# Kernel tuning notes

Hardware: AMD Instinct MI355X
Metric: run time of the kernel (lower is better)

## Reference

```python
import jax, jax.numpy as jnp
import numpy as np

T, B, N = 512, 256, 128


def setup_inputs() -> dict:
    key = jax.random.key(0)
    k1, k2, k3, k4, k5, k6 = jax.random.split(key, 6)
    emit = jax.random.normal(k1, (T, B, N), dtype=jnp.float32)
    target = jax.random.randint(k2, (T, B), 0, N, dtype=jnp.int32)
    # monotone mask: each sequence has length in [T//2, T]
    lengths = jax.random.randint(k3, (B,), T // 2, T + 1, dtype=jnp.int32)
    mask = jnp.arange(T, dtype=jnp.int32)[:, None] < lengths[None, :]
    trans = 0.1 * jax.random.normal(k4, (N, N), dtype=jnp.float32)
    strans = 0.1 * jax.random.normal(k5, (N,), dtype=jnp.float32)
    etrans = 0.1 * jax.random.normal(k6, (N,), dtype=jnp.float32)
    return {"emit": emit, "target": target, "mask": mask,
            "trans": trans, "strans": strans, "etrans": etrans}


def _crf_nll(emit, trans, strans, etrans, target, mask):
    t_len, b, n = emit.shape

    # ---- logZ: forward algorithm (sequential scan over time) ----
    def step(alpha, inp):
        emit_i, mask_i = inp  # [B,N], [B]
        # scores[b, j, k] = alpha[b, j] + trans[j, k] + emit_i[b, k]
        scores = jax.nn.logsumexp(
            alpha[:, :, None] + trans[None, :, :] + emit_i[:, None, :], axis=1)
        alpha = jnp.where(mask_i[:, None], scores, alpha)
        return alpha, None

    alpha0 = strans[None, :] + emit[0]  # [B,N]
    alpha, _ = jax.lax.scan(step, alpha0, (emit[1:], mask[1:]))
    logZ = jax.nn.logsumexp(alpha + etrans[None, :], axis=1).sum()

    # ---- gold score ----
    emit_sc = jnp.take_along_axis(emit, target[:, :, None], axis=2)[..., 0]  # [T,B]
    trans_sc = trans[target[:-1], target[1:]]  # [T-1,B]
    scores = emit_sc.at[1:].add(trans_sc)
    score = jnp.where(mask, scores, 0.0).sum()
    ends = mask.sum(axis=0) - 1  # [B]
    score = score + strans[target[0]].sum()
    score = score + etrans[target[ends, jnp.arange(b)]].sum()

    return (logZ - score) / b


def reference(emit, target, mask, trans, strans, etrans):
    return _crf_nll(emit, trans, strans, etrans, target, mask)
```

## Files before the change

### kernel.cpp

```cpp
#include <hip/hip_runtime.h>

#define T_LEN 512
#define B_SZ  256
#define N_ST  128

#if defined(__has_builtin)
# if __has_builtin(__builtin_amdgcn_fdot2_f32_bf16)
#  define HAVE_DOT2 1
# endif
#endif
#ifndef HAVE_DOT2
# define HAVE_DOT2 0
#endif

typedef unsigned int uint32;
typedef __bf16 bf16x2 __attribute__((ext_vector_type(2)));
typedef float f2v __attribute__((ext_vector_type(2)));
typedef uint4 __attribute__((may_alias)) uint4a;

__device__ __forceinline__ uint32 bf16rn(float f) {
    uint32 u = __builtin_bit_cast(uint32, f);
    u += 0x7fffu + ((u >> 16) & 1u);
    return u >> 16;
}
__device__ __forceinline__ uint32 pack2(float lo, float hi) {
    return bf16rn(lo) | (bf16rn(hi) << 16);
}
__device__ __forceinline__ uint32 cvtpk(float lo, float hi) {
    uint32 r;
    asm("v_cvt_pk_bf16_f32 %0, %1, %2" : "=v"(r) : "v"(lo), "v"(hi));
    return r;
}
__device__ __forceinline__ float readlane0(float v) {
    return __builtin_bit_cast(float, (uint32)__builtin_amdgcn_readlane(__builtin_bit_cast(int, v), 0));
}
__device__ __forceinline__ float dot2b(uint32 a, uint32 b, float c) {
#if HAVE_DOT2
    return __builtin_amdgcn_fdot2_f32_bf16(__builtin_bit_cast(bf16x2, a),
                                           __builtin_bit_cast(bf16x2, b), c, false);
#else
    float alo = __builtin_bit_cast(float, a << 16);
    float ahi = __builtin_bit_cast(float, a & 0xffff0000u);
    float blo = __builtin_bit_cast(float, b << 16);
    float bhi = __builtin_bit_cast(float, b & 0xffff0000u);
    return fmaf(ahi, bhi, fmaf(alo, blo, c));
#endif
}


__global__ __launch_bounds__(64) void lengths_kernel(const unsigned char* __restrict__ mask_raw,
                                                     int* __restrict__ lens) {
    int b = blockIdx.x;
    int l = threadIdx.x;
    unsigned char b1 = mask_raw[1], b2 = mask_raw[2];
    int mode = (b1 != 0) ? 0 : ((b2 != 0) ? 2 : 1);
    int cnt = 0;
    if (mode == 0) {
        #pragma unroll
        for (int k = 0; k < 8; ++k) cnt += (mask_raw[(l * 8 + k) * B_SZ + b] != 0);
    } else if (mode == 1) {
        const int* m = (const int*)mask_raw;
        #pragma unroll
        for (int k = 0; k < 8; ++k) cnt += (m[(l * 8 + k) * B_SZ + b] != 0);
    } else {
        const float* m = (const float*)mask_raw;
        #pragma unroll
        for (int k = 0; k < 8; ++k) cnt += (m[(l * 8 + k) * B_SZ + b] != 0.0f);
    }
    #pragma unroll
    for (int off = 1; off < 64; off <<= 1) cnt += __shfl_xor(cnt, off);
    if (l == 0) lens[b] = cnt;
}

__global__ void __attribute__((amdgpu_flat_work_group_size(128, 128), amdgpu_waves_per_eu(1, 1)))
forward_kernel(
        const float* __restrict__ emit,
        const float* __restrict__ trans,
        const float* __restrict__ strans,
        const float* __restrict__ etrans,
        const int* __restrict__ lens,
        float* __restrict__ logZ_out) {
    const int b   = blockIdx.x;
    const int tid = threadIdx.x;
    const int wid = tid >> 6;
    const int l   = tid & 63;
    const int c0  = 2 * l, c1 = 2 * l + 1;

    __shared__ alignas(16) uint32 a32[64];
    __shared__ alignas(16) uint32 z32[64];
    __shared__ float meetA[N_ST], meetY[N_ST];
    __shared__ float maccSh[2], red2[2];

    const int len = lens[b];
    const int m = (len - 1 < 256) ? (len - 1) : 256;
    const float* eb = emit + (size_t)b * N_ST;
    const size_t TS2 = (size_t)B_SZ * N_ST / 2;
    const f2v* ebv = (const f2v*)eb;

    if (wid == 0) {
        uint32 EA[64], EB[64];
        #pragma unroll
        for (int p = 0; p < 64; ++p) {
            EA[p] = pack2(__expf(trans[(2 * p) * N_ST + c0]), __expf(trans[(2 * p + 1) * N_ST + c0]));
            EB[p] = pack2(__expf(trans[(2 * p) * N_ST + c1]), __expf(trans[(2 * p + 1) * N_ST + c1]));
        }
        float aA = __expf(strans[c0] + eb[c0]);
        float aB = __expf(strans[c1] + eb[c1]);
        a32[l] = pack2(aA, aB);
        float Macc = 0.f, inv = 1.0f;
        #define EIDX(T) ((size_t)(((T) <= m) ? (T) : m) * TS2 + l)
        f2v p0 = ebv[EIDX(1)];
        f2v p1 = ebv[EIDX(2)];
        f2v p2 = ebv[EIDX(3)];
        f2v p3 = ebv[EIDX(4)];
        for (int t = 1; t <= m; ++t) {
            const f2v pn = ebv[EIDX(t + 4)];
            const float ee0 = __expf(p0.x), ee1 = __expf(p0.y);
            float A0 = 0, A1 = 0, A2 = 0, A3 = 0, B0 = 0, B1 = 0, B2 = 0, B3 = 0;
            const uint4a* aw = (const uint4a*)a32;
            #pragma unroll
            for (int q = 0; q < 16; ++q) {
                const uint4 w = aw[q];
                A0 = dot2b(w.x, EA[4 * q + 0], A0);  B0 = dot2b(w.x, EB[4 * q + 0], B0);
                A1 = dot2b(w.y, EA[4 * q + 1], A1);  B1 = dot2b(w.y, EB[4 * q + 1], B1);
                A2 = dot2b(w.z, EA[4 * q + 2], A2);  B2 = dot2b(w.z, EB[4 * q + 2], B2);
                A3 = dot2b(w.w, EA[4 * q + 3], A3);  B3 = dot2b(w.w, EB[4 * q + 3], B3);
            }
            const float rA = (A0 + A1) + (A2 + A3);
            const float rB = (B0 + B1) + (B2 + B3);
            Macc -= __logf(inv);
            aA = ee0 * rA * inv;
            aB = ee1 * rB * inv;
            a32[l] = cvtpk(aA, aB);
            inv = __builtin_amdgcn_rcpf(readlane0(rA));
            p0 = p1; p1 = p2; p2 = p3; p3 = pn;
        }
        #undef EIDX
        meetA[c0] = aA; meetA[c1] = aB;
        if (l == 0) maccSh[0] = Macc;
    } else {
        uint32 RA[64], RB[64];
        #pragma unroll
        for (int p = 0; p < 64; ++p) {
            RA[p] = pack2(__expf(trans[c0 * N_ST + 2 * p]), __expf(trans[c0 * N_ST + 2 * p + 1]));
            RB[p] = pack2(__expf(trans[c1 * N_ST + 2 * p]), __expf(trans[c1 * N_ST + 2 * p + 1]));
        }
        float y0 = __expf(etrans[c0]);
        float y1 = __expf(etrans[c1]);
        float Maccb = 0.f, invb = 1.0f;
        const int t0 = len - 1;
        #define EIDXB(T) ((size_t)(((T) > m) ? (T) : (m + 1)) * TS2 + l)
        f2v p0 = ebv[EIDXB(t0)];
        f2v p1 = ebv[EIDXB(t0 - 1)];
        f2v p2 = ebv[EIDXB(t0 - 2)];
        f2v p3 = ebv[EIDXB(t0 - 3)];
        for (int t = t0; t > m; --t) {
            const f2v pn = ebv[EIDXB(t - 4)];
            const float ee0 = __expf(p0.x), ee1 = __expf(p0.y);
            z32[l] = cvtpk(ee0 * y0, ee1 * y1);
            float R0 = 0, R1 = 0, R2 = 0, R3 = 0, S0 = 0, S1 = 0, S2 = 0, S3 = 0;
            const uint4a* zw = (const uint4a*)z32;
            #pragma unroll
            for (int q = 0; q < 16; ++q) {
                const uint4 w = zw[q];
                R0 = dot2b(w.x, RA[4 * q + 0], R0);  S0 = dot2b(w.x, RB[4 * q + 0], S0);
                R1 = dot2b(w.y, RA[4 * q + 1], R1);  S1 = dot2b(w.y, RB[4 * q + 1], S1);
                R2 = dot2b(w.z, RA[4 * q + 2], R2);  S2 = dot2b(w.z, RB[4 * q + 2], S2);
                R3 = dot2b(w.w, RA[4 * q + 3], R3);  S3 = dot2b(w.w, RB[4 * q + 3], S3);
            }
            const float rR = (R0 + R1) + (R2 + R3);
            const float rS = (S0 + S1) + (S2 + S3);
            Maccb -= __logf(invb);
            y0 = rR * invb;
            y1 = rS * invb;
            invb = __builtin_amdgcn_rcpf(readlane0(rR));
            p0 = p1; p1 = p2; p2 = p3; p3 = pn;
        }
        #undef EIDXB
        meetY[c0] = y0; meetY[c1] = y1;
        if (l == 0) maccSh[1] = Maccb;
    }

    __syncthreads();
    float v = meetA[tid] * meetY[tid];
    #pragma unroll
    for (int off = 1; off < 64; off <<= 1) v += __shfl_xor(v, off);
    if (l == 0) red2[wid] = v;
    __syncthreads();
    if (tid == 0) logZ_out[b] = maccSh[0] + maccSh[1] + __logf(red2[0] + red2[1]);
}

__global__ __launch_bounds__(128) void score_kernel(
        const float* __restrict__ emit,
        const int* __restrict__ target,
        const float* __restrict__ trans,
        const float* __restrict__ strans,
        const float* __restrict__ etrans,
        const int* __restrict__ lens,
        float* __restrict__ score_out) {
    const int b   = blockIdx.x;
    const int tid = threadIdx.x;
    const int len = lens[b];
    float local = 0.f;
    for (int t = tid; t < len; t += 128) {
        int tgt = target[t * B_SZ + b];
        float v = emit[(size_t)t * (B_SZ * N_ST) + b * N_ST + tgt];
        if (t > 0) v += trans[target[(t - 1) * B_SZ + b] * N_ST + tgt];
        local += v;
    }
    if (tid == 0) {
        local += strans[target[b]];
        local += etrans[target[(len - 1) * B_SZ + b]];
    }
    #pragma unroll
    for (int off = 1; off < 64; off <<= 1) local += __shfl_xor(local, off);
    __shared__ float partial[2];
    if ((tid & 63) == 0) partial[tid >> 6] = local;
    __syncthreads();
    if (tid == 0) score_out[b] = partial[0] + partial[1];
}

__global__ __launch_bounds__(256) void finalize_kernel(
        const float* __restrict__ logZ,
        const float* __restrict__ score,
        float* __restrict__ out) {
    int tid = threadIdx.x;
    float v = logZ[tid] - score[tid];
    #pragma unroll
    for (int off = 1; off < 64; off <<= 1) v += __shfl_xor(v, off);
    __shared__ float p[4];
    if ((tid & 63) == 0) p[tid >> 6] = v;
    __syncthreads();
    if (tid == 0) out[0] = (p[0] + p[1] + p[2] + p[3]) / 256.0f;
}

extern "C" void kernel_launch(void* const* d_in, const int* in_sizes, int n_in,
                              void* d_out, int out_size, void* d_ws, size_t ws_size,
                              hipStream_t stream) {
    const float*         emit   = (const float*)d_in[0];
    const int*           target = (const int*)d_in[1];
    const unsigned char* mask   = (const unsigned char*)d_in[2];
    const float*         trans  = (const float*)d_in[3];
    const float*         strans = (const float*)d_in[4];
    const float*         etrans = (const float*)d_in[5];

    float* ws     = (float*)d_ws;
    float* logZb  = ws;
    float* scoreb = ws + 256;
    int*   lens   = (int*)(ws + 512);

    lengths_kernel<<<B_SZ, 64, 0, stream>>>(mask, lens);
    forward_kernel<<<B_SZ, 128, 0, stream>>>(emit, trans, strans, etrans, lens, logZb);
    score_kernel<<<B_SZ, 128, 0, stream>>>(emit, target, trans, strans, etrans, lens, scoreb);
    finalize_kernel<<<1, 256, 0, stream>>>(logZb, scoreb, (float*)d_out);
}
```

Measured before the change: 123.2 us.

## Split CRF forward recursion into independent forward and backward halves per sequence

The partition function is now computed by two independent single-wave blocks per sequence. One runs the forward recursion over the first half of the timesteps and the other runs the backward recursion over the rest. A small combine kernel then takes the dot product of the two message vectors. This removes the intra-block cross-wave synchronisation of the fused two-wave kernel and shortens each serial chain to about half the length. The cost is an extra kernel launch, more blocks, and a dependence on workspace size, with the old fused kernel kept as a fallback.

```diff
diff --git a/kernel.cpp b/kernel.cpp
--- a/kernel.cpp
+++ b/kernel.cpp
@@ -47,6 +47,7 @@
 #endif
 }
 
+#define WS_NEED_BYTES (66816 * 4)
 
 __global__ __launch_bounds__(64) void lengths_kernel(const unsigned char* __restrict__ mask_raw,
                                                      int* __restrict__ lens) {
@@ -72,8 +73,130 @@
     if (l == 0) lens[b] = cnt;
 }
 
+__global__ void __attribute__((amdgpu_flat_work_group_size(64, 64), amdgpu_waves_per_eu(1, 1)))
+forward_split(
+        const float* __restrict__ emit,
+        const float* __restrict__ trans,
+        const float* __restrict__ strans,
+        const float* __restrict__ etrans,
+        const int* __restrict__ lens,
+        float* __restrict__ wsMF, float* __restrict__ wsMB,
+        float* __restrict__ wsU, float* __restrict__ wsY) {
+    const int b   = blockIdx.x >> 1;
+    const int dir = blockIdx.x & 1;
+    const int l   = threadIdx.x;
+    const int c0  = 2 * l, c1 = 2 * l + 1;
+
+    __shared__ alignas(16) uint32 s32[64];
+
+    const int len = lens[b];
+    const int m = (len - 1 < 256) ? (len - 1) : 256;
+    const float* eb = emit + (size_t)b * N_ST;
+    const size_t TS2 = (size_t)B_SZ * N_ST / 2;
+    const f2v* ebv = (const f2v*)eb;
+
+    if (dir == 0) {
+        uint32 EA[64], EB[64];
+        #pragma unroll
+        for (int p = 0; p < 64; ++p) {
+            EA[p] = pack2(__expf(trans[(2 * p) * N_ST + c0]), __expf(trans[(2 * p + 1) * N_ST + c0]));
+            EB[p] = pack2(__expf(trans[(2 * p) * N_ST + c1]), __expf(trans[(2 * p + 1) * N_ST + c1]));
+        }
+        float aA = __expf(strans[c0] + eb[c0]);
+        float aB = __expf(strans[c1] + eb[c1]);
+        s32[l] = pack2(aA, aB);
+        float Macc = 0.f, inv = 1.0f;
+        #define EIDX(T) ((size_t)(((T) <= m) ? (T) : m) * TS2 + l)
+        f2v p0 = ebv[EIDX(1)];
+        f2v p1 = ebv[EIDX(2)];
+        f2v p2 = ebv[EIDX(3)];
+        f2v p3 = ebv[EIDX(4)];
+        for (int t = 1; t <= m; ++t) {
+            const f2v pn = ebv[EIDX(t + 4)];
+            const float ee0 = __expf(p0.x), ee1 = __expf(p0.y);
+            float A0 = 0, A1 = 0, A2 = 0, A3 = 0, B0 = 0, B1 = 0, B2 = 0, B3 = 0;
+            const uint4a* aw = (const uint4a*)s32;
+            #pragma unroll
+            for (int q = 0; q < 16; ++q) {
+                const uint4 w = aw[q];
+                A0 = dot2b(w.x, EA[4 * q + 0], A0);  B0 = dot2b(w.x, EB[4 * q + 0], B0);
+                A1 = dot2b(w.y, EA[4 * q + 1], A1);  B1 = dot2b(w.y, EB[4 * q + 1], B1);
+                A2 = dot2b(w.z, EA[4 * q + 2], A2);  B2 = dot2b(w.z, EB[4 * q + 2], B2);
+                A3 = dot2b(w.w, EA[4 * q + 3], A3);  B3 = dot2b(w.w, EB[4 * q + 3], B3);
+            }
+            const float rA = (A0 + A1) + (A2 + A3);
+            const float rB = (B0 + B1) + (B2 + B3);
+            Macc -= __logf(inv);
+            aA = ee0 * rA * inv;
+            aB = ee1 * rB * inv;
+            s32[l] = cvtpk(aA, aB);
+            inv = __builtin_amdgcn_rcpf(readlane0(rA));
+            p0 = p1; p1 = p2; p2 = p3; p3 = pn;
+        }
+        #undef EIDX
+        wsU[b * N_ST + c0] = aA;
+        wsU[b * N_ST + c1] = aB;
+        if (l == 0) wsMF[b] = Macc;
+    } else {
+        uint32 RA[64], RB[64];
+        #pragma unroll
+        for (int p = 0; p < 64; ++p) {
+            RA[p] = pack2(__expf(trans[c0 * N_ST + 2 * p]), __expf(trans[c0 * N_ST + 2 * p + 1]));
+            RB[p] = pack2(__expf(trans[c1 * N_ST + 2 * p]), __expf(trans[c1 * N_ST + 2 * p + 1]));
+        }
+        float y0 = __expf(etrans[c0]);
+        float y1 = __expf(etrans[c1]);
+        float Maccb = 0.f, invb = 1.0f;
+        const int t0 = len - 1;
+        #define EIDXB(T) ((size_t)(((T) > m) ? (T) : (m + 1)) * TS2 + l)
+        f2v p0 = ebv[EIDXB(t0)];
+        f2v p1 = ebv[EIDXB(t0 - 1)];
+        f2v p2 = ebv[EIDXB(t0 - 2)];
+        f2v p3 = ebv[EIDXB(t0 - 3)];
+        for (int t = t0; t > m; --t) {
+            const f2v pn = ebv[EIDXB(t - 4)];
+            const float ee0 = __expf(p0.x), ee1 = __expf(p0.y);
+            s32[l] = cvtpk(ee0 * y0, ee1 * y1);
+            float R0 = 0, R1 = 0, R2 = 0, R3 = 0, S0 = 0, S1 = 0, S2 = 0, S3 = 0;
+            const uint4a* zw = (const uint4a*)s32;
+            #pragma unroll
+            for (int q = 0; q < 16; ++q) {
+                const uint4 w = zw[q];
+                R0 = dot2b(w.x, RA[4 * q + 0], R0);  S0 = dot2b(w.x, RB[4 * q + 0], S0);
+                R1 = dot2b(w.y, RA[4 * q + 1], R1);  S1 = dot2b(w.y, RB[4 * q + 1], S1);
+                R2 = dot2b(w.z, RA[4 * q + 2], R2);  S2 = dot2b(w.z, RB[4 * q + 2], S2);
+                R3 = dot2b(w.w, RA[4 * q + 3], R3);  S3 = dot2b(w.w, RB[4 * q + 3], S3);
+            }
+            const float rR = (R0 + R1) + (R2 + R3);
+            const float rS = (S0 + S1) + (S2 + S3);
+            Maccb -= __logf(invb);
+            y0 = rR * invb;
+            y1 = rS * invb;
+            invb = __builtin_amdgcn_rcpf(readlane0(rR));
+            p0 = p1; p1 = p2; p2 = p3; p3 = pn;
+        }
+        #undef EIDXB
+        wsY[b * N_ST + c0] = y0;
+        wsY[b * N_ST + c1] = y1;
+        if (l == 0) wsMB[b] = Maccb;
+    }
+}
+
+__global__ __launch_bounds__(64) void combine_kernel(
+        const float* __restrict__ wsU, const float* __restrict__ wsY,
+        const float* __restrict__ wsMF, const float* __restrict__ wsMB,
+        float* __restrict__ logZ) {
+    const int b = blockIdx.x;
+    const int l = threadIdx.x;
+    float v = wsU[b * N_ST + l] * wsY[b * N_ST + l]
+            + wsU[b * N_ST + l + 64] * wsY[b * N_ST + l + 64];
+    #pragma unroll
+    for (int off = 1; off < 64; off <<= 1) v += __shfl_xor(v, off);
+    if (l == 0) logZ[b] = wsMF[b] + wsMB[b] + __logf(v);
+}
+
 __global__ void __attribute__((amdgpu_flat_work_group_size(128, 128), amdgpu_waves_per_eu(1, 1)))
-forward_kernel(
+forward_fused(
         const float* __restrict__ emit,
         const float* __restrict__ trans,
         const float* __restrict__ strans,
@@ -248,9 +371,19 @@
     float* logZb  = ws;
     float* scoreb = ws + 256;
     int*   lens   = (int*)(ws + 512);
+    float* wsMF   = ws + 768;
+    float* wsMB   = ws + 1024;
+    float* wsU    = ws + 1280;
+    float* wsY    = ws + 34048;
 
     lengths_kernel<<<B_SZ, 64, 0, stream>>>(mask, lens);
-    forward_kernel<<<B_SZ, 128, 0, stream>>>(emit, trans, strans, etrans, lens, logZb);
+    if (ws_size >= (size_t)WS_NEED_BYTES) {
+        forward_split<<<2 * B_SZ, 64, 0, stream>>>(emit, trans, strans, etrans, lens,
+                                                   wsMF, wsMB, wsU, wsY);
+        combine_kernel<<<B_SZ, 64, 0, stream>>>(wsU, wsY, wsMF, wsMB, logZb);
+    } else {
+        forward_fused<<<B_SZ, 128, 0, stream>>>(emit, trans, strans, etrans, lens, logZb);
+    }
     score_kernel<<<B_SZ, 128, 0, stream>>>(emit, target, trans, strans, etrans, lens, scoreb);
     finalize_kernel<<<1, 256, 0, stream>>>(logZb, scoreb, (float*)d_out);
 }
```

After: 128.2 us. 1.04x slower.

## Fuse length, forward-backward and gold-score kernels into one kernel

Applied to the files above, without the earlier changes.

The lengths kernel and score kernel are folded into the forward kernel. Each wave now computes the sequence length itself, and a third wave per block computes the gold score alongside the two forward/backward recurrence waves. This removes two kernel launches and their dependency gaps. In exchange, the block grows to 192 threads, every wave redundantly counts the mask, and the score wave's global loads may contend with the latency-critical recurrence waves.

```diff
diff --git a/kernel.cpp b/kernel.cpp
--- a/kernel.cpp
+++ b/kernel.cpp
@@ -47,11 +47,7 @@
 #endif
 }
 
-
-__global__ __launch_bounds__(64) void lengths_kernel(const unsigned char* __restrict__ mask_raw,
-                                                     int* __restrict__ lens) {
-    int b = blockIdx.x;
-    int l = threadIdx.x;
+__device__ __forceinline__ int wave_len(const unsigned char* __restrict__ mask_raw, int b, int l) {
     unsigned char b1 = mask_raw[1], b2 = mask_raw[2];
     int mode = (b1 != 0) ? 0 : ((b2 != 0) ? 2 : 1);
     int cnt = 0;
@@ -59,27 +55,30 @@
         #pragma unroll
         for (int k = 0; k < 8; ++k) cnt += (mask_raw[(l * 8 + k) * B_SZ + b] != 0);
     } else if (mode == 1) {
-        const int* m = (const int*)mask_raw;
-        #pragma unroll
-        for (int k = 0; k < 8; ++k) cnt += (m[(l * 8 + k) * B_SZ + b] != 0);
+        const int* mm = (const int*)mask_raw;
+        #pragma unroll
+        for (int k = 0; k < 8; ++k) cnt += (mm[(l * 8 + k) * B_SZ + b] != 0);
     } else {
-        const float* m = (const float*)mask_raw;
-        #pragma unroll
-        for (int k = 0; k < 8; ++k) cnt += (m[(l * 8 + k) * B_SZ + b] != 0.0f);
+        const float* mm = (const float*)mask_raw;
+        #pragma unroll
+        for (int k = 0; k < 8; ++k) cnt += (mm[(l * 8 + k) * B_SZ + b] != 0.0f);
     }
     #pragma unroll
     for (int off = 1; off < 64; off <<= 1) cnt += __shfl_xor(cnt, off);
-    if (l == 0) lens[b] = cnt;
-}
-
-__global__ void __attribute__((amdgpu_flat_work_group_size(128, 128), amdgpu_waves_per_eu(1, 1)))
-forward_kernel(
+    return cnt;
+}
+
+
+__global__ void __attribute__((amdgpu_flat_work_group_size(192, 192), amdgpu_waves_per_eu(1, 1)))
+crf_fused_kernel(
         const float* __restrict__ emit,
+        const unsigned char* __restrict__ mask_raw,
+        const int* __restrict__ target,
         const float* __restrict__ trans,
         const float* __restrict__ strans,
         const float* __restrict__ etrans,
-        const int* __restrict__ lens,
-        float* __restrict__ logZ_out) {
+        float* __restrict__ logZ_out,
+        float* __restrict__ score_out) {
     const int b   = blockIdx.x;
     const int tid = threadIdx.x;
     const int wid = tid >> 6;
@@ -91,7 +90,7 @@
     __shared__ float meetA[N_ST], meetY[N_ST];
     __shared__ float maccSh[2], red2[2];
 
-    const int len = lens[b];
+    const int len = wave_len(mask_raw, b, l);
     const int m = (len - 1 < 256) ? (len - 1) : 256;
     const float* eb = emit + (size_t)b * N_ST;
     const size_t TS2 = (size_t)B_SZ * N_ST / 2;
@@ -138,7 +137,7 @@
         #undef EIDX
         meetA[c0] = aA; meetA[c1] = aB;
         if (l == 0) maccSh[0] = Macc;
-    } else {
+    } else if (wid == 1) {
         uint32 RA[64], RB[64];
         #pragma unroll
         for (int p = 0; p < 64; ++p) {
@@ -179,45 +178,32 @@
         #undef EIDXB
         meetY[c0] = y0; meetY[c1] = y1;
         if (l == 0) maccSh[1] = Maccb;
+    } else {
+        float local = 0.f;
+        for (int t = l; t < len; t += 64) {
+            int tgt = target[t * B_SZ + b];
+            float v = emit[(size_t)t * (B_SZ * N_ST) + b * N_ST + tgt];
+            if (t > 0) v += trans[target[(t - 1) * B_SZ + b] * N_ST + tgt];
+            local += v;
+        }
+        if (l == 0) {
+            local += strans[target[b]];
+            local += etrans[target[(len - 1) * B_SZ + b]];
+        }
+        #pragma unroll
+        for (int off = 1; off < 64; off <<= 1) local += __shfl_xor(local, off);
+        if (l == 0) score_out[b] = local;
     }
 
     __syncthreads();
-    float v = meetA[tid] * meetY[tid];
-    #pragma unroll
-    for (int off = 1; off < 64; off <<= 1) v += __shfl_xor(v, off);
-    if (l == 0) red2[wid] = v;
+    if (wid < 2) {
+        float v = meetA[tid] * meetY[tid];
+        #pragma unroll
+        for (int off = 1; off < 64; off <<= 1) v += __shfl_xor(v, off);
+        if (l == 0) red2[wid] = v;
+    }
     __syncthreads();
     if (tid == 0) logZ_out[b] = maccSh[0] + maccSh[1] + __logf(red2[0] + red2[1]);
-}
-
-__global__ __launch_bounds__(128) void score_kernel(
-        const float* __restrict__ emit,
-        const int* __restrict__ target,
-        const float* __restrict__ trans,
-        const float* __restrict__ strans,
-        const float* __restrict__ etrans,
-        const int* __restrict__ lens,
-        float* __restrict__ score_out) {
-    const int b   = blockIdx.x;
-    const int tid = threadIdx.x;
-    const int len = lens[b];
-    float local = 0.f;
-    for (int t = tid; t < len; t += 128) {
-        int tgt = target[t * B_SZ + b];
-        float v = emit[(size_t)t * (B_SZ * N_ST) + b * N_ST + tgt];
-        if (t > 0) v += trans[target[(t - 1) * B_SZ + b] * N_ST + tgt];
-        local += v;
-    }
-    if (tid == 0) {
-        local += strans[target[b]];
-        local += etrans[target[(len - 1) * B_SZ + b]];
-    }
-    #pragma unroll
-    for (int off = 1; off < 64; off <<= 1) local += __shfl_xor(local, off);
-    __shared__ float partial[2];
-    if ((tid & 63) == 0) partial[tid >> 6] = local;
-    __syncthreads();
-    if (tid == 0) score_out[b] = partial[0] + partial[1];
 }
 
 __global__ __launch_bounds__(256) void finalize_kernel(
@@ -247,10 +233,8 @@
     float* ws     = (float*)d_ws;
     float* logZb  = ws;
     float* scoreb = ws + 256;
-    int*   lens   = (int*)(ws + 512);
-
-    lengths_kernel<<<B_SZ, 64, 0, stream>>>(mask, lens);
-    forward_kernel<<<B_SZ, 128, 0, stream>>>(emit, trans, strans, etrans, lens, logZb);
-    score_kernel<<<B_SZ, 128, 0, stream>>>(emit, target, trans, strans, etrans, lens, scoreb);
+
+    crf_fused_kernel<<<B_SZ, 192, 0, stream>>>(emit, mask, target, trans, strans, etrans,
+                                               logZb, scoreb);
     finalize_kernel<<<1, 256, 0, stream>>>(logZb, scoreb, (float*)d_out);
 }
```

Measured after the change: 117.5 us, median of 2. -4.6%, faster.
